# Optimization experiments

Measured on AMD Instinct MI355X. Metric: run time of the kernel, lower is better.

Reference implementation:

```python
import jax, jax.numpy as jnp
import numpy as np

D_MODEL = 1024
NUM_HEADS = 16
DEPTH = D_MODEL // NUM_HEADS


def setup_inputs() -> dict:
    key = jax.random.key(0)
    ks = jax.random.split(key, 9)
    B, S = 2, 2048
    scale = 1.0 / np.sqrt(D_MODEL)
    x = jax.random.normal(ks[0], (B, S, D_MODEL), dtype=jnp.float32)
    wq = jax.random.normal(ks[1], (D_MODEL, D_MODEL), dtype=jnp.float32) * scale
    wk = jax.random.normal(ks[2], (D_MODEL, D_MODEL), dtype=jnp.float32) * scale
    wv = jax.random.normal(ks[3], (D_MODEL, D_MODEL), dtype=jnp.float32) * scale
    wo = jax.random.normal(ks[4], (D_MODEL, D_MODEL), dtype=jnp.float32) * scale
    bq = jnp.zeros((D_MODEL,), dtype=jnp.float32)
    bk = jnp.zeros((D_MODEL,), dtype=jnp.float32)
    bv = jnp.zeros((D_MODEL,), dtype=jnp.float32)
    bo = jnp.zeros((D_MODEL,), dtype=jnp.float32)
    return {"x": x, "wq": wq, "bq": bq, "wk": wk, "bk": bk,
            "wv": wv, "bv": bv, "wo": wo, "bo": bo}


def _split_heads(t):
    # [B, S, D] -> [B, H, S, depth]
    B, S, _ = t.shape
    return t.reshape(B, S, NUM_HEADS, DEPTH).transpose(0, 2, 1, 3)


def reference(x, wq, bq, wk, bk, wv, bv, wo, bo):
    q = _split_heads(x @ wq + bq)
    k = _split_heads(x @ wk + bk)
    v = _split_heads(x @ wv + bv)
    # scaled dot-product attention with materialized [B,H,S,S] scores
    logits = jnp.einsum("bhqd,bhkd->bhqk", q, k) / jnp.sqrt(
        jnp.asarray(DEPTH, dtype=x.dtype))
    attn = jax.nn.softmax(logits, axis=-1)
    out = jnp.einsum("bhqk,bhkd->bhqd", attn, v)
    B, _, S, _ = out.shape
    concat = out.transpose(0, 2, 1, 3).reshape(B, S, D_MODEL)
    return concat @ wo + bo
```

## Files before the change

kernel.cpp:

```cpp
#include <hip/hip_runtime.h>
#include <hip/hip_bf16.h>
#include <stdint.h>

typedef unsigned short u16;
typedef __attribute__((ext_vector_type(8))) short short8;
typedef __attribute__((ext_vector_type(4))) float f32x4;

__device__ __forceinline__ float bf2f(u16 u) {
    union { uint32_t u; float f; } v; v.u = ((uint32_t)u) << 16; return v.f;
}
__device__ __forceinline__ u16 f2bf(float f) {
    union { float f; uint32_t u; } v; v.f = f;
    uint32_t r = (v.u + 0x7fffu + ((v.u >> 16) & 1u)) >> 16;
    return (u16)r;
}
__device__ __forceinline__ uint32_t pkbf(float a, float b) {
    union { __hip_bfloat162 h; uint32_t w; } u;
    u.h = __float22bfloat162_rn(float2{a, b});
    return u.w;
}
__device__ __forceinline__ void store_out(u16* p, float v) { *p = f2bf(v); }
__device__ __forceinline__ void store_out(float* p, float v) { *p = v; }

__device__ __forceinline__ void async_ld16(const u16* g, u16* l) {
    __builtin_amdgcn_global_load_lds(
        (const __attribute__((address_space(1))) void*)g,
        (__attribute__((address_space(3))) void*)l, 16, 0, 0);
}

__global__ void prep(const float* __restrict__ x,
                     const float* __restrict__ w0, const float* __restrict__ w1,
                     const float* __restrict__ w2, const float* __restrict__ w3,
                     u16* __restrict__ xb, u16* __restrict__ wT,
                     u16* __restrict__ woT) {
    const int z = blockIdx.z;
    __shared__ u16 tile[32][33];
    if (z == 3 || z == 4) {
        int blk = (z - 3) * 1024 + blockIdx.y * 32 + blockIdx.x;
        int tid = threadIdx.y * 32 + threadIdx.x;
        int i = (blk * 256 + tid) * 8;
        float4 a = *(const float4*)(x + i);
        float4 b = *(const float4*)(x + i + 4);
        union { uint32_t w[4]; uint4 v; } o;
        o.w[0] = pkbf(a.x, a.y); o.w[1] = pkbf(a.z, a.w);
        o.w[2] = pkbf(b.x, b.y); o.w[3] = pkbf(b.z, b.w);
        *(uint4*)(xb + i) = o.v;
        return;
    }
    const float* in = (z == 0) ? w0 : (z == 1) ? w1 : (z == 2) ? w2 : w3;
    u16* o = (z < 3) ? (wT + (size_t)z * 1024 * 1024) : woT;
    int xx = blockIdx.x * 32 + threadIdx.x;
    int y0 = blockIdx.y * 32;
#pragma unroll
    for (int j = threadIdx.y; j < 32; j += 8)
        tile[j][threadIdx.x] = f2bf(in[(size_t)(y0 + j) * 1024 + xx]);
    __syncthreads();
    int ox = blockIdx.y * 32 + threadIdx.x;
    int oy0 = blockIdx.x * 32;
#pragma unroll
    for (int j = threadIdx.y; j < 32; j += 8)
        o[(size_t)(oy0 + j) * 1024 + ox] = tile[threadIdx.x][j];
}

__global__ void transpose1(const float* __restrict__ w, u16* __restrict__ out) {
    __shared__ u16 tile[32][33];
    int x = blockIdx.x * 32 + threadIdx.x;
    int y0 = blockIdx.y * 32;
#pragma unroll
    for (int j = threadIdx.y; j < 32; j += 8)
        tile[j][threadIdx.x] = f2bf(w[(size_t)(y0 + j) * 1024 + x]);
    __syncthreads();
    int ox = blockIdx.y * 32 + threadIdx.x;
    int oy0 = blockIdx.x * 32;
#pragma unroll
    for (int j = threadIdx.y; j < 32; j += 8)
        out[(size_t)(oy0 + j) * 1024 + ox] = tile[threadIdx.x][j];
}

#define GBM 128
#define GBN 128
#define GBK 32

template <typename OutT>
__global__ __launch_bounds__(256) void gemm_bt(
    const u16* __restrict__ A, int lda,
    const u16* __restrict__ BT, int ldb,
    const float* __restrict__ bias0, const float* __restrict__ bias1,
    const float* __restrict__ bias2,
    OutT* __restrict__ C, int ldc, int K) {
    __shared__ __align__(16) u16 As[2][GBM * GBK];
    __shared__ __align__(16) u16 Bs[2][GBN * GBK];

    const int tid = threadIdx.x;
    const int wave = tid >> 6, lane = tid & 63;
    const int quad = lane >> 4, l16 = lane & 15;
    const int wr = wave >> 1, wc = wave & 1;

    int bx = blockIdx.x, by = blockIdx.y;
    if (gridDim.x == 24 && gridDim.y == 32) {
        const int wgid = blockIdx.x + blockIdx.y * 24;
        const int xcd = wgid & 7, t = wgid >> 3;
        bx = (xcd & 1) * 12 + t % 12;
        by = (xcd >> 1) * 8 + t / 12;
    }
    const int m0 = by * GBM, n0 = bx * GBN;

    const int seg = n0 >> 10;
    const float* bsel = (seg == 0) ? bias0 : (seg == 1) ? bias1 : bias2;

    f32x4 acc[4][4] = {};

    const int srow = tid >> 2;
    const int scol = (tid & 3) * 8;
    const u16* Ag0 = A + (size_t)(m0 + srow) * lda + scol;
    const u16* Ag1 = Ag0 + (size_t)64 * lda;
    const u16* Bg0 = BT + (size_t)(n0 + srow) * ldb + scol;
    const u16* Bg1 = Bg0 + (size_t)64 * ldb;
    const int woff = wave << 9;

    async_ld16(Ag0, As[0] + woff);
    async_ld16(Ag1, As[0] + woff + 64 * GBK);
    async_ld16(Bg0, Bs[0] + woff);
    async_ld16(Bg1, Bs[0] + woff + 64 * GBK);

    int cur = 0;
    for (int kb = 0; kb < K; kb += GBK) {
        __syncthreads();

        if (kb + GBK < K) {
            const int nxt = cur ^ 1;
            async_ld16(Ag0 + kb + GBK, As[nxt] + woff);
            async_ld16(Ag1 + kb + GBK, As[nxt] + woff + 64 * GBK);
            async_ld16(Bg0 + kb + GBK, Bs[nxt] + woff);
            async_ld16(Bg1 + kb + GBK, Bs[nxt] + woff + 64 * GBK);
        }

        short8 af[4], bf[4];
#pragma unroll
        for (int mt = 0; mt < 4; mt++)
            af[mt] = *(const short8*)(As[cur] + (wr * 64 + mt * 16 + l16) * GBK + quad * 8);
#pragma unroll
        for (int nt = 0; nt < 4; nt++)
            bf[nt] = *(const short8*)(Bs[cur] + (wc * 64 + nt * 16 + l16) * GBK + quad * 8);
#pragma unroll
        for (int mt = 0; mt < 4; mt++)
#pragma unroll
            for (int nt = 0; nt < 4; nt++)
                acc[mt][nt] = __builtin_amdgcn_mfma_f32_16x16x32_bf16(
                    af[mt], bf[nt], acc[mt][nt], 0, 0, 0);
        cur ^= 1;
    }

#pragma unroll
    for (int nt = 0; nt < 4; nt++) {
        int col = n0 + wc * 64 + nt * 16 + l16;
        float bv = bsel[col & 1023];
#pragma unroll
        for (int mt = 0; mt < 4; mt++) {
            int row = m0 + wr * 64 + mt * 16 + quad * 4;
#pragma unroll
            for (int r = 0; r < 4; r++)
                store_out(&C[(size_t)(row + r) * ldc + col], acc[mt][nt][r] + bv);
        }
    }
}

__global__ __launch_bounds__(256) void gemm_bt64(
    const u16* __restrict__ A, int lda,
    const u16* __restrict__ BT, int ldb,
    const float* __restrict__ bias,
    float* __restrict__ C, int ldc, int K) {
    __shared__ __align__(16) u16 As[2][64 * GBK];
    __shared__ __align__(16) u16 Bs[2][128 * GBK];

    const int tid = threadIdx.x;
    const int wave = tid >> 6, lane = tid & 63;
    const int quad = lane >> 4, l16 = lane & 15;

    int bx = blockIdx.x, by = blockIdx.y;
    if (gridDim.x == 8 && gridDim.y == 64) {
        const int wgid = blockIdx.x + blockIdx.y * 8;
        const int xcd = wgid & 7, t = wgid >> 3;
        bx = t & 7;
        by = (xcd << 3) + (t >> 3);
    }
    const int m0 = by * 64, n0 = bx * 128;

    f32x4 acc[4][2] = {};

    const int srow = tid >> 2;
    const int scol = (tid & 3) * 8;
    const u16* Ag0 = A + (size_t)(m0 + srow) * lda + scol;
    const u16* Bg0 = BT + (size_t)(n0 + srow) * ldb + scol;
    const u16* Bg1 = Bg0 + (size_t)64 * ldb;
    const int woff = wave << 9;

    async_ld16(Ag0, As[0] + woff);
    async_ld16(Bg0, Bs[0] + woff);
    async_ld16(Bg1, Bs[0] + woff + 64 * GBK);

    int cur = 0;
    for (int kb = 0; kb < K; kb += GBK) {
        __syncthreads();

        if (kb + GBK < K) {
            const int nxt = cur ^ 1;
            async_ld16(Ag0 + kb + GBK, As[nxt] + woff);
            async_ld16(Bg0 + kb + GBK, Bs[nxt] + woff);
            async_ld16(Bg1 + kb + GBK, Bs[nxt] + woff + 64 * GBK);
        }

        short8 af[4], bf[2];
#pragma unroll
        for (int mt = 0; mt < 4; mt++)
            af[mt] = *(const short8*)(As[cur] + (mt * 16 + l16) * GBK + quad * 8);
#pragma unroll
        for (int nt = 0; nt < 2; nt++)
            bf[nt] = *(const short8*)(Bs[cur] + (wave * 32 + nt * 16 + l16) * GBK + quad * 8);
#pragma unroll
        for (int mt = 0; mt < 4; mt++)
#pragma unroll
            for (int nt = 0; nt < 2; nt++)
                acc[mt][nt] = __builtin_amdgcn_mfma_f32_16x16x32_bf16(
                    af[mt], bf[nt], acc[mt][nt], 0, 0, 0);
        cur ^= 1;
    }

#pragma unroll
    for (int nt = 0; nt < 2; nt++) {
        int col = n0 + wave * 32 + nt * 16 + l16;
        float bv = bias[col & 1023];
#pragma unroll
        for (int mt = 0; mt < 4; mt++) {
            int row = m0 + mt * 16 + quad * 4;
#pragma unroll
            for (int r = 0; r < 4; r++)
                C[(size_t)(row + r) * ldc + col] = acc[mt][nt][r] + bv;
        }
    }
}

#define SEQ 2048
#define BQT 128
#define BKV 128
#define LDK 72
#define LDKV 136

__global__ __launch_bounds__(256) void attn(u16* __restrict__ QKV) {
    __shared__ __align__(16) u16 Ks[BKV * LDK];
    __shared__ __align__(16) u16 Vs[64 * LDKV];

    const int tid = threadIdx.x;
    const int wave = tid >> 6, lane = tid & 63;
    const int quad = lane >> 4, l16 = lane & 15;
    const int h = blockIdx.y, bb = blockIdx.z;
    const int q0 = blockIdx.x * BQT;
    const size_t tok0 = (size_t)bb * SEQ;

    const u16* Qb = QKV + tok0 * 3072 + h * 64;
    const u16* Kb = QKV + tok0 * 3072 + 1024 + h * 64;
    const u16* Vb = QKV + tok0 * 3072 + 2048 + h * 64;

    const float cs = 0.18033688011112042f;

    int qr[2];
    qr[0] = q0 + wave * 16 + l16;
    qr[1] = qr[0] + 64;
    short8 aq[2][2];
#pragma unroll
    for (int s = 0; s < 2; s++) {
        union { short8 v; u16 u[8]; uint32_t w[4]; } qa, qb;
        qa.v = *(const short8*)(Qb + (size_t)qr[s] * 3072 + quad * 8);
        qb.v = *(const short8*)(Qb + (size_t)qr[s] * 3072 + 32 + quad * 8);
#pragma unroll
        for (int j = 0; j < 4; j++) {
            qa.w[j] = pkbf(bf2f(qa.u[2 * j]) * cs, bf2f(qa.u[2 * j + 1]) * cs);
            qb.w[j] = pkbf(bf2f(qb.u[2 * j]) * cs, bf2f(qb.u[2 * j + 1]) * cs);
        }
        aq[s][0] = qa.v; aq[s][1] = qb.v;
    }

    f32x4 o[2][4] = {};
    f32x4 o_l[2] = {};

    const short8 vone = {16256, 16256, 16256, 16256,
                         16256, 16256, 16256, 16256};

    const int srow = tid >> 2;
    const int scc = (tid & 3) * 16;
    const int pr = tid & 63;
    const int dg = wave;

    const u16* kg = Kb + (size_t)srow * 3072 + scc;
    const u16* vg = Vb + (size_t)(2 * pr) * 3072 + dg * 16;

    const int kvb = 2 * pr;
    const int kvp = (kvb & 96) | (((kvb >> 2) & 3) << 3) |
                    (((kvb >> 4) & 1) << 2) | (kvb & 3);

    uint4 k0r = *(const uint4*)(kg);
    uint4 k1r = *(const uint4*)(kg + 8);
    uint4 k2r = *(const uint4*)(kg + (size_t)64 * 3072);
    uint4 k3r = *(const uint4*)(kg + (size_t)64 * 3072 + 8);
    uint4 va0 = *(const uint4*)(vg);
    uint4 va1 = *(const uint4*)(vg + 8);
    uint4 vb0 = *(const uint4*)(vg + 3072);
    uint4 vb1 = *(const uint4*)(vg + 3072 + 8);

    for (int j0 = 0; j0 < SEQ; j0 += BKV) {
        *(uint4*)(Ks + srow * LDK + scc) = k0r;
        *(uint4*)(Ks + srow * LDK + scc + 8) = k1r;
        *(uint4*)(Ks + (srow + 64) * LDK + scc) = k2r;
        *(uint4*)(Ks + (srow + 64) * LDK + scc + 8) = k3r;
        {
            union { uint4 v[2]; u16 u[16]; } a, b;
            a.v[0] = va0; a.v[1] = va1; b.v[0] = vb0; b.v[1] = vb1;
#pragma unroll
            for (int j = 0; j < 16; j++) {
                uint32_t w = (uint32_t)a.u[j] | ((uint32_t)b.u[j] << 16);
                *(uint32_t*)(Vs + (dg * 16 + j) * LDKV + kvp) = w;
            }
        }
        __syncthreads();

        if (j0 + BKV < SEQ) {
            size_t off = (size_t)(j0 + BKV) * 3072;
            k0r = *(const uint4*)(kg + off);
            k1r = *(const uint4*)(kg + off + 8);
            k2r = *(const uint4*)(kg + off + (size_t)64 * 3072);
            k3r = *(const uint4*)(kg + off + (size_t)64 * 3072 + 8);
            va0 = *(const uint4*)(vg + off);
            va1 = *(const uint4*)(vg + off + 8);
            vb0 = *(const uint4*)(vg + off + 3072);
            vb1 = *(const uint4*)(vg + off + 3072 + 8);
        }

        f32x4 st[2][8];
        __builtin_amdgcn_s_setprio(1);
#pragma unroll
        for (int kkt = 0; kkt < 8; kkt++) {
            f32x4 s0 = {}, s1 = {};
#pragma unroll
            for (int k2 = 0; k2 < 2; k2++) {
                short8 ak = *(const short8*)(Ks + (kkt * 16 + l16) * LDK + k2 * 32 + quad * 8);
                s0 = __builtin_amdgcn_mfma_f32_16x16x32_bf16(ak, aq[0][k2], s0, 0, 0, 0);
                s1 = __builtin_amdgcn_mfma_f32_16x16x32_bf16(ak, aq[1][k2], s1, 0, 0, 0);
            }
            st[0][kkt] = s0; st[1][kkt] = s1;
        }
        __builtin_amdgcn_s_setprio(0);

#pragma unroll
        for (int s = 0; s < 2; s++)
#pragma unroll
            for (int kkt = 0; kkt < 8; kkt++)
#pragma unroll
                for (int r = 0; r < 4; r++)
                    st[s][kkt][r] = __builtin_amdgcn_exp2f(st[s][kkt][r]);

        __builtin_amdgcn_s_setprio(1);
#pragma unroll
        for (int tt = 0; tt < 4; tt++) {
            union { uint32_t w[4]; short8 v; } bp0, bp1;
            bp0.w[0] = pkbf(st[0][2 * tt][0], st[0][2 * tt][1]);
            bp0.w[1] = pkbf(st[0][2 * tt][2], st[0][2 * tt][3]);
            bp0.w[2] = pkbf(st[0][2 * tt + 1][0], st[0][2 * tt + 1][1]);
            bp0.w[3] = pkbf(st[0][2 * tt + 1][2], st[0][2 * tt + 1][3]);
            bp1.w[0] = pkbf(st[1][2 * tt][0], st[1][2 * tt][1]);
            bp1.w[1] = pkbf(st[1][2 * tt][2], st[1][2 * tt][3]);
            bp1.w[2] = pkbf(st[1][2 * tt + 1][0], st[1][2 * tt + 1][1]);
            bp1.w[3] = pkbf(st[1][2 * tt + 1][2], st[1][2 * tt + 1][3]);

            o_l[0] = __builtin_amdgcn_mfma_f32_16x16x32_bf16(vone, bp0.v, o_l[0], 0, 0, 0);
            o_l[1] = __builtin_amdgcn_mfma_f32_16x16x32_bf16(vone, bp1.v, o_l[1], 0, 0, 0);
#pragma unroll
            for (int dt = 0; dt < 4; dt++) {
                short8 av = *(const short8*)(Vs + (dt * 16 + l16) * LDKV +
                                             tt * 32 + quad * 8);
                o[0][dt] = __builtin_amdgcn_mfma_f32_16x16x32_bf16(av, bp0.v, o[0][dt], 0, 0, 0);
                o[1][dt] = __builtin_amdgcn_mfma_f32_16x16x32_bf16(av, bp1.v, o[1][dt], 0, 0, 0);
            }
        }
        __builtin_amdgcn_s_setprio(0);

        __syncthreads();
    }

#pragma unroll
    for (int s = 0; s < 2; s++) {
        const float inv_l = 1.0f / o_l[s][0];
        u16* orow = QKV + (tok0 + qr[s]) * 3072 + h * 64;
#pragma unroll
        for (int dt = 0; dt < 4; dt++) {
            uint32_t w0 = pkbf(o[s][dt][0] * inv_l, o[s][dt][1] * inv_l);
            uint32_t w1 = pkbf(o[s][dt][2] * inv_l, o[s][dt][3] * inv_l);
            uint2 w = {w0, w1};
            *(uint2*)(orow + dt * 16 + quad * 4) = w;
        }
    }
}

extern "C" void kernel_launch(void* const* d_in, const int* in_sizes, int n_in,
                              void* d_out, int out_size, void* d_ws, size_t ws_size,
                              hipStream_t stream) {
    const float* x  = (const float*)d_in[0];
    const float* wq = (const float*)d_in[1];
    const float* bq = (const float*)d_in[2];
    const float* wk = (const float*)d_in[3];
    const float* bk = (const float*)d_in[4];
    const float* wv = (const float*)d_in[5];
    const float* bv = (const float*)d_in[6];
    const float* wo = (const float*)d_in[7];
    const float* bo = (const float*)d_in[8];
    (void)in_sizes; (void)n_in; (void)out_size;

    u16* QKV = (u16*)d_ws;
    u16* wT  = QKV + (size_t)4096 * 3072;
    u16* xb  = wT + (size_t)3 * 1024 * 1024;
    u16* woT = xb;
    u16* woT2 = xb + (size_t)4096 * 1024;

    const size_t need = ((size_t)4096 * 3072 + (size_t)4 * 1024 * 1024 +
                         (size_t)4096 * 1024) * sizeof(u16);
    const bool fused = (ws_size >= need);

    if (fused) {
        prep<<<dim3(32, 32, 6), dim3(32, 8), 0, stream>>>(x, wq, wk, wv, wo,
                                                          xb, wT, woT2);
        gemm_bt<u16><<<dim3(24, 32), 256, 0, stream>>>(xb, 1024, wT, 1024,
                                                       bq, bk, bv, QKV, 3072, 1024);
        attn<<<dim3(16, 16, 2), 256, 0, stream>>>(QKV);
        gemm_bt64<<<dim3(8, 64), 256, 0, stream>>>(QKV, 3072, woT2, 1024, bo,
                                                   (float*)d_out, 1024, 1024);
    } else {
        prep<<<dim3(32, 32, 5), dim3(32, 8), 0, stream>>>(x, wq, wk, wv, wo,
                                                          xb, wT, woT2);
        gemm_bt<u16><<<dim3(24, 32), 256, 0, stream>>>(xb, 1024, wT, 1024,
                                                       bq, bk, bv, QKV, 3072, 1024);
        transpose1<<<dim3(32, 32), dim3(32, 8), 0, stream>>>(wo, woT);
        attn<<<dim3(16, 16, 2), 256, 0, stream>>>(QKV);
        gemm_bt64<<<dim3(8, 64), 256, 0, stream>>>(QKV, 3072, woT, 1024, bo,
                                                   (float*)d_out, 1024, 1024);
    }
}
```

Baseline: 193.9 us.

## Double KV tile to 256 and swizzle attention blocks across XCDs

Raises the attention KV tile from 128 to 256 rows, processed as two 128-row halves per tile, which halves the number of __syncthreads barriers and LDS staging rounds. It also remaps the linear block index so that blocks sharing a head's K/V land on the same XCD, aiming for better L2 reuse. In exchange the kernel uses more LDS and more prefetch registers per block, which can lower occupancy.

New measurement: 229.0 us. +18.1%, slower.

```diff
diff --git a/kernel.cpp b/kernel.cpp
--- a/kernel.cpp
+++ b/kernel.cpp
@@ -242,9 +242,9 @@
 
 #define SEQ 2048
 #define BQT 128
-#define BKV 128
+#define BKV 256
 #define LDK 72
-#define LDKV 136
+#define LDKV 264
 
 __global__ __launch_bounds__(256) void attn(u16* __restrict__ QKV) {
     __shared__ __align__(16) u16 Ks[BKV * LDK];
@@ -253,8 +253,13 @@
     const int tid = threadIdx.x;
     const int wave = tid >> 6, lane = tid & 63;
     const int quad = lane >> 4, l16 = lane & 15;
-    const int h = blockIdx.y, bb = blockIdx.z;
-    const int q0 = blockIdx.x * BQT;
+
+    const int lin = blockIdx.x + blockIdx.y * 16 + blockIdx.z * 256;
+    const int xcd = lin & 7, tswz = lin >> 3;
+    const int h  = (xcd >> 1) | ((tswz & 3) << 2);
+    const int qb = ((xcd & 1) << 3) | ((tswz >> 2) & 7);
+    const int bb = tswz >> 5;
+    const int q0 = qb * BQT;
     const size_t tok0 = (size_t)bb * SEQ;
 
     const u16* Qb = QKV + tok0 * 3072 + h * 64;
@@ -269,15 +274,15 @@
     short8 aq[2][2];
 #pragma unroll
     for (int s = 0; s < 2; s++) {
-        union { short8 v; u16 u[8]; uint32_t w[4]; } qa, qb;
+        union { short8 v; u16 u[8]; uint32_t w[4]; } qa, qc;
         qa.v = *(const short8*)(Qb + (size_t)qr[s] * 3072 + quad * 8);
-        qb.v = *(const short8*)(Qb + (size_t)qr[s] * 3072 + 32 + quad * 8);
+        qc.v = *(const short8*)(Qb + (size_t)qr[s] * 3072 + 32 + quad * 8);
 #pragma unroll
         for (int j = 0; j < 4; j++) {
             qa.w[j] = pkbf(bf2f(qa.u[2 * j]) * cs, bf2f(qa.u[2 * j + 1]) * cs);
-            qb.w[j] = pkbf(bf2f(qb.u[2 * j]) * cs, bf2f(qb.u[2 * j + 1]) * cs);
-        }
-        aq[s][0] = qa.v; aq[s][1] = qb.v;
+            qc.w[j] = pkbf(bf2f(qc.u[2 * j]) * cs, bf2f(qc.u[2 * j + 1]) * cs);
+        }
+        aq[s][0] = qa.v; aq[s][1] = qc.v;
     }
 
     f32x4 o[2][4] = {};
@@ -298,90 +303,113 @@
     const int kvp = (kvb & 96) | (((kvb >> 2) & 3) << 3) |
                     (((kvb >> 4) & 1) << 2) | (kvb & 3);
 
-    uint4 k0r = *(const uint4*)(kg);
-    uint4 k1r = *(const uint4*)(kg + 8);
-    uint4 k2r = *(const uint4*)(kg + (size_t)64 * 3072);
-    uint4 k3r = *(const uint4*)(kg + (size_t)64 * 3072 + 8);
-    uint4 va0 = *(const uint4*)(vg);
-    uint4 va1 = *(const uint4*)(vg + 8);
-    uint4 vb0 = *(const uint4*)(vg + 3072);
-    uint4 vb1 = *(const uint4*)(vg + 3072 + 8);
+    uint4 kr[8];
+    uint4 vr[8];
+#pragma unroll
+    for (int i = 0; i < 4; i++) {
+        kr[2 * i]     = *(const uint4*)(kg + (size_t)(64 * i) * 3072);
+        kr[2 * i + 1] = *(const uint4*)(kg + (size_t)(64 * i) * 3072 + 8);
+    }
+    vr[0] = *(const uint4*)(vg);
+    vr[1] = *(const uint4*)(vg + 8);
+    vr[2] = *(const uint4*)(vg + 3072);
+    vr[3] = *(const uint4*)(vg + 3072 + 8);
+    vr[4] = *(const uint4*)(vg + (size_t)128 * 3072);
+    vr[5] = *(const uint4*)(vg + (size_t)128 * 3072 + 8);
+    vr[6] = *(const uint4*)(vg + (size_t)129 * 3072);
+    vr[7] = *(const uint4*)(vg + (size_t)129 * 3072 + 8);
 
     for (int j0 = 0; j0 < SEQ; j0 += BKV) {
-        *(uint4*)(Ks + srow * LDK + scc) = k0r;
-        *(uint4*)(Ks + srow * LDK + scc + 8) = k1r;
-        *(uint4*)(Ks + (srow + 64) * LDK + scc) = k2r;
-        *(uint4*)(Ks + (srow + 64) * LDK + scc + 8) = k3r;
+#pragma unroll
+        for (int i = 0; i < 4; i++) {
+            *(uint4*)(Ks + (srow + 64 * i) * LDK + scc) = kr[2 * i];
+            *(uint4*)(Ks + (srow + 64 * i) * LDK + scc + 8) = kr[2 * i + 1];
+        }
         {
             union { uint4 v[2]; u16 u[16]; } a, b;
-            a.v[0] = va0; a.v[1] = va1; b.v[0] = vb0; b.v[1] = vb1;
+            a.v[0] = vr[0]; a.v[1] = vr[1]; b.v[0] = vr[2]; b.v[1] = vr[3];
 #pragma unroll
             for (int j = 0; j < 16; j++) {
                 uint32_t w = (uint32_t)a.u[j] | ((uint32_t)b.u[j] << 16);
                 *(uint32_t*)(Vs + (dg * 16 + j) * LDKV + kvp) = w;
             }
+            a.v[0] = vr[4]; a.v[1] = vr[5]; b.v[0] = vr[6]; b.v[1] = vr[7];
+#pragma unroll
+            for (int j = 0; j < 16; j++) {
+                uint32_t w = (uint32_t)a.u[j] | ((uint32_t)b.u[j] << 16);
+                *(uint32_t*)(Vs + (dg * 16 + j) * LDKV + kvp + 128) = w;
+            }
         }
         __syncthreads();
 
         if (j0 + BKV < SEQ) {
-            size_t off = (size_t)(j0 + BKV) * 3072;
-            k0r = *(const uint4*)(kg + off);
-            k1r = *(const uint4*)(kg + off + 8);
-            k2r = *(const uint4*)(kg + off + (size_t)64 * 3072);
-            k3r = *(const uint4*)(kg + off + (size_t)64 * 3072 + 8);
-            va0 = *(const uint4*)(vg + off);
-            va1 = *(const uint4*)(vg + off + 8);
-            vb0 = *(const uint4*)(vg + off + 3072);
-            vb1 = *(const uint4*)(vg + off + 3072 + 8);
-        }
-
-        f32x4 st[2][8];
-        __builtin_amdgcn_s_setprio(1);
-#pragma unroll
-        for (int kkt = 0; kkt < 8; kkt++) {
-            f32x4 s0 = {}, s1 = {};
-#pragma unroll
-            for (int k2 = 0; k2 < 2; k2++) {
-                short8 ak = *(const short8*)(Ks + (kkt * 16 + l16) * LDK + k2 * 32 + quad * 8);
-                s0 = __builtin_amdgcn_mfma_f32_16x16x32_bf16(ak, aq[0][k2], s0, 0, 0, 0);
-                s1 = __builtin_amdgcn_mfma_f32_16x16x32_bf16(ak, aq[1][k2], s1, 0, 0, 0);
+            const size_t off = (size_t)(j0 + BKV) * 3072;
+#pragma unroll
+            for (int i = 0; i < 4; i++) {
+                kr[2 * i]     = *(const uint4*)(kg + off + (size_t)(64 * i) * 3072);
+                kr[2 * i + 1] = *(const uint4*)(kg + off + (size_t)(64 * i) * 3072 + 8);
             }
-            st[0][kkt] = s0; st[1][kkt] = s1;
-        }
-        __builtin_amdgcn_s_setprio(0);
-
-#pragma unroll
-        for (int s = 0; s < 2; s++)
-#pragma unroll
-            for (int kkt = 0; kkt < 8; kkt++)
-#pragma unroll
-                for (int r = 0; r < 4; r++)
-                    st[s][kkt][r] = __builtin_amdgcn_exp2f(st[s][kkt][r]);
-
-        __builtin_amdgcn_s_setprio(1);
-#pragma unroll
-        for (int tt = 0; tt < 4; tt++) {
-            union { uint32_t w[4]; short8 v; } bp0, bp1;
-            bp0.w[0] = pkbf(st[0][2 * tt][0], st[0][2 * tt][1]);
-            bp0.w[1] = pkbf(st[0][2 * tt][2], st[0][2 * tt][3]);
-            bp0.w[2] = pkbf(st[0][2 * tt + 1][0], st[0][2 * tt + 1][1]);
-            bp0.w[3] = pkbf(st[0][2 * tt + 1][2], st[0][2 * tt + 1][3]);
-            bp1.w[0] = pkbf(st[1][2 * tt][0], st[1][2 * tt][1]);
-            bp1.w[1] = pkbf(st[1][2 * tt][2], st[1][2 * tt][3]);
-            bp1.w[2] = pkbf(st[1][2 * tt + 1][0], st[1][2 * tt + 1][1]);
-            bp1.w[3] = pkbf(st[1][2 * tt + 1][2], st[1][2 * tt + 1][3]);
-
-            o_l[0] = __builtin_amdgcn_mfma_f32_16x16x32_bf16(vone, bp0.v, o_l[0], 0, 0, 0);
-            o_l[1] = __builtin_amdgcn_mfma_f32_16x16x32_bf16(vone, bp1.v, o_l[1], 0, 0, 0);
-#pragma unroll
-            for (int dt = 0; dt < 4; dt++) {
-                short8 av = *(const short8*)(Vs + (dt * 16 + l16) * LDKV +
-                                             tt * 32 + quad * 8);
-                o[0][dt] = __builtin_amdgcn_mfma_f32_16x16x32_bf16(av, bp0.v, o[0][dt], 0, 0, 0);
-                o[1][dt] = __builtin_amdgcn_mfma_f32_16x16x32_bf16(av, bp1.v, o[1][dt], 0, 0, 0);
+            vr[0] = *(const uint4*)(vg + off);
+            vr[1] = *(const uint4*)(vg + off + 8);
+            vr[2] = *(const uint4*)(vg + off + 3072);
+            vr[3] = *(const uint4*)(vg + off + 3072 + 8);
+            vr[4] = *(const uint4*)(vg + off + (size_t)128 * 3072);
+            vr[5] = *(const uint4*)(vg + off + (size_t)128 * 3072 + 8);
+            vr[6] = *(const uint4*)(vg + off + (size_t)129 * 3072);
+            vr[7] = *(const uint4*)(vg + off + (size_t)129 * 3072 + 8);
+        }
+
+#pragma unroll
+        for (int hf = 0; hf < 2; hf++) {
+            f32x4 st[2][8];
+            __builtin_amdgcn_s_setprio(1);
+#pragma unroll
+            for (int kkt = 0; kkt < 8; kkt++) {
+                f32x4 s0 = {}, s1 = {};
+#pragma unroll
+                for (int k2 = 0; k2 < 2; k2++) {
+                    short8 ak = *(const short8*)(Ks + (hf * 128 + kkt * 16 + l16) * LDK +
+                                                 k2 * 32 + quad * 8);
+                    s0 = __builtin_amdgcn_mfma_f32_16x16x32_bf16(ak, aq[0][k2], s0, 0, 0, 0);
+                    s1 = __builtin_amdgcn_mfma_f32_16x16x32_bf16(ak, aq[1][k2], s1, 0, 0, 0);
+                }
+                st[0][kkt] = s0; st[1][kkt] = s1;
             }
-        }
-        __builtin_amdgcn_s_setprio(0);
+            __builtin_amdgcn_s_setprio(0);
+
+#pragma unroll
+            for (int s = 0; s < 2; s++)
+#pragma unroll
+                for (int kkt = 0; kkt < 8; kkt++)
+#pragma unroll
+                    for (int r = 0; r < 4; r++)
+                        st[s][kkt][r] = __builtin_amdgcn_exp2f(st[s][kkt][r]);
+
+            __builtin_amdgcn_s_setprio(1);
+#pragma unroll
+            for (int tt = 0; tt < 4; tt++) {
+                union { uint32_t w[4]; short8 v; } bp0, bp1;
+                bp0.w[0] = pkbf(st[0][2 * tt][0], st[0][2 * tt][1]);
+                bp0.w[1] = pkbf(st[0][2 * tt][2], st[0][2 * tt][3]);
+                bp0.w[2] = pkbf(st[0][2 * tt + 1][0], st[0][2 * tt + 1][1]);
+                bp0.w[3] = pkbf(st[0][2 * tt + 1][2], st[0][2 * tt + 1][3]);
+                bp1.w[0] = pkbf(st[1][2 * tt][0], st[1][2 * tt][1]);
+                bp1.w[1] = pkbf(st[1][2 * tt][2], st[1][2 * tt][3]);
+                bp1.w[2] = pkbf(st[1][2 * tt + 1][0], st[1][2 * tt + 1][1]);
+                bp1.w[3] = pkbf(st[1][2 * tt + 1][2], st[1][2 * tt + 1][3]);
+
+                o_l[0] = __builtin_amdgcn_mfma_f32_16x16x32_bf16(vone, bp0.v, o_l[0], 0, 0, 0);
+                o_l[1] = __builtin_amdgcn_mfma_f32_16x16x32_bf16(vone, bp1.v, o_l[1], 0, 0, 0);
+#pragma unroll
+                for (int dt = 0; dt < 4; dt++) {
+                    short8 av = *(const short8*)(Vs + (dt * 16 + l16) * LDKV +
+                                                 hf * 128 + tt * 32 + quad * 8);
+                    o[0][dt] = __builtin_amdgcn_mfma_f32_16x16x32_bf16(av, bp0.v, o[0][dt], 0, 0, 0);
+                    o[1][dt] = __builtin_amdgcn_mfma_f32_16x16x32_bf16(av, bp1.v, o[1][dt], 0, 0, 0);
+                }
+            }
+            __builtin_amdgcn_s_setprio(0);
+        }
 
         __syncthreads();
     }
```
